# Kernel tuning notes

Hardware: AMD Instinct MI355X
Metric: run time of the kernel (lower is better)

## Reference

```python
import jax, jax.numpy as jnp
import numpy as np


def _conv(x, w, pad):
    return jax.lax.conv_general_dilated(
        x, w, (1, 1), [(pad, pad), (pad, pad)],
        dimension_numbers=('NCHW', 'OIHW', 'NCHW'))


def _avgpool2(x):
    B, C, H, W = x.shape
    return x.reshape(B, C, H // 2, 2, W // 2, 2).mean(axis=(3, 5))


def setup_inputs() -> dict:
    key = jax.random.key(0)
    ks = jax.random.split(key, 10)
    B = 1024
    x = jax.random.uniform(ks[0], (B, 1, 28, 28), jnp.float32)
    # depthwise-separable conv params (in=1 -> depthwise is a plain 3x3 conv)
    dw_w = jax.random.normal(ks[1], (1, 1, 3, 3), jnp.float32) * 0.3
    pw_w = jax.random.normal(ks[2], (32, 1, 1, 1), jnp.float32) * 0.3
    pw_b = jax.random.normal(ks[3], (32,), jnp.float32) * 0.05
    # fixed 4-qubit entangling unitary (real orthogonal 16x16), stand-in for tq.RandomLayer(n_ops=8)
    U = jnp.asarray(np.linalg.qr(np.random.default_rng(0).standard_normal((16, 16)))[0],
                    jnp.float32)
    fus_w = jax.random.normal(ks[4], (128, 36, 3, 3), jnp.float32) * (1.0 / np.sqrt(36 * 9))
    fus_b = jax.random.normal(ks[5], (128,), jnp.float32) * 0.05
    F = 128 * 7 * 7
    cls_w = jax.random.normal(ks[6], (10, F), jnp.float32) * (1.0 / np.sqrt(F))
    cls_b = jax.random.normal(ks[7], (10,), jnp.float32) * 0.05
    reg_w = jax.random.normal(ks[8], (1, F), jnp.float32) * (1.0 / np.sqrt(F))
    reg_b = jax.random.normal(ks[9], (1,), jnp.float32) * 0.05
    return {'x': x, 'dw_w': dw_w, 'pw_w': pw_w, 'pw_b': pw_b, 'U': U,
            'fus_w': fus_w, 'fus_b': fus_b, 'cls_w': cls_w, 'cls_b': cls_b,
            'reg_w': reg_w, 'reg_b': reg_b}


def _quantum_patches(x, U):
    # x: (B,1,28,28) -> 14x14 grid of 2x2 patches, 4 RY angles per patch
    B = x.shape[0]
    p = x.reshape(B, 14, 2, 14, 2).transpose(0, 1, 3, 2, 4).reshape(B, 14, 14, 4)
    h = 0.5 * p
    a = jnp.stack([jnp.cos(h), jnp.sin(h)], axis=-1)       # (B,14,14,4,2)
    # RY-encoded product state |psi> = kron over 4 wires -> 16 real amplitudes
    amp = jnp.einsum('...i,...j,...k,...l->...ijkl',
                     a[..., 0, :], a[..., 1, :], a[..., 2, :], a[..., 3, :]
                     ).reshape(B, 14, 14, 16)
    state = amp @ U.T                                       # entangling layer
    probs = state * state
    idx = jnp.arange(16)
    # PauliZ expectation per wire; wire 0 is the most significant bit
    signs = 1.0 - 2.0 * (((idx[None, :] >> (3 - jnp.arange(4)[:, None])) & 1)
                         .astype(jnp.float32))              # (4,16)
    meas = probs @ signs.T                                  # (B,14,14,4)
    # replicate torch.cat(patches,dim=1).view(B,4,14,14): flat row-major then reshape
    return meas.reshape(B, 14 * 14 * 4).reshape(B, 4, 14, 14)


def reference(x, dw_w, pw_w, pw_b, U, fus_w, fus_b, cls_w, cls_b, reg_w, reg_b):
    B = x.shape[0]
    out_ds = _conv(_conv(x, dw_w, 1), pw_w, 0) + pw_b[None, :, None, None]  # (B,32,28,28)
    out_q = _quantum_patches(x, U)                                          # (B,4,14,14)
    out = jnp.concatenate([_avgpool2(out_ds), out_q], axis=1)               # (B,36,14,14)
    out = jax.nn.relu(_conv(out, fus_w, 1) + fus_b[None, :, None, None])    # (B,128,14,14)
    out = _avgpool2(out)                                                    # (B,128,7,7)
    flat = out.reshape(B, -1)
    logits = flat @ cls_w.T + cls_b
    aux = flat @ reg_w.T + reg_b
    return (logits, aux)
```

## Files before the change

kernel.cpp:

```cpp
#include <hip/hip_runtime.h>
#include <math.h>


typedef __bf16 bf16x8 __attribute__((ext_vector_type(8)));
typedef __bf16 bf16x4 __attribute__((ext_vector_type(4)));
typedef float  f32x16 __attribute__((ext_vector_type(16)));

union Pack8 { __bf16 h[8]; uint4 v; };
union QPair { struct { bf16x4 lo, hi; } p; bf16x8 v; };

__global__ __launch_bounds__(256) void prep(
    const float* __restrict__ fus_w,
    const float* __restrict__ cls_w,
    const float* __restrict__ reg_w,
    __bf16* __restrict__ bfrag,
    float* __restrict__ clsTT)
{
    const int gid = blockIdx.x * 256 + threadIdx.x;
    if (gid < 43008) {
        const int j    = gid & 7;
        const int frag = gid >> 3;
        const int lane = frag & 63;
        const int rest = frag >> 6;
        const int m  = rest % 21;
        const int nt = rest / 21;
        const int n  = nt * 32 + (lane & 31);
        const int hk = lane >> 5;
        float v;
        if (m < 18) {
            const int t = m >> 1, ks = m & 1;
            const int ic = ks * 16 + hk * 8 + j;
            v = fus_w[n * 324 + ic * 9 + t];
        } else {
            const int ps = m - 18;
            const int k  = hk * 8 + j;
            const int tap = ps * 4 + (k >> 2);
            const int ch  = k & 3;
            v = (tap < 9) ? fus_w[n * 324 + (32 + ch) * 9 + tap] : 0.f;
        }
        bfrag[gid] = (__bf16)v;
    } else if (gid < 43008 + 86016) {
        const int e   = gid - 43008;
        const int kk  = e % 12;
        const int r0  = e / 12;
        const int l31 = r0 & 31;
        const int r1  = r0 >> 5;
        const int hk  = r1 & 1;
        const int r2  = r1 >> 1;
        const int q   = r2 & 3;
        const int r3  = r2 >> 2;
        const int mt  = r3 % 7;
        const int nt  = r3 / 7;
        const int oc   = nt * 32 + l31;
        const int cell = mt * 8 + q * 2 + hk;
        float v = 0.f;
        if (cell < 49 && kk < 11) {
            const int f = oc * 49 + cell;
            v = (kk < 10) ? cls_w[kk * 6272 + f] : reg_w[f];
        }
        clsTT[e] = v;
    }
}

__device__ __forceinline__ void patch_work(
    const int tid, const float* __restrict__ xs, __bf16* __restrict__ actT,
    __bf16* __restrict__ Qt,
    const float* __restrict__ dw_w, const float* __restrict__ pw_w,
    const float* __restrict__ pw_b, const float* __restrict__ U)
{
    if (tid >= 196) return;
    const int i = tid / 14, j = tid % 14;
    const int Y = 2 * i, X = 2 * j;

    float w9[9];
    #pragma unroll
    for (int t = 0; t < 9; ++t) w9[t] = dw_w[t];
    float dsum = 0.f;
    #pragma unroll
    for (int dy = 0; dy < 2; ++dy) {
        #pragma unroll
        for (int dx = 0; dx < 2; ++dx) {
            const int cy = Y + dy, cx = X + dx;
            #pragma unroll
            for (int ky = 0; ky < 3; ++ky) {
                const int yy = cy + ky - 1;
                if (yy < 0 || yy > 27) continue;
                #pragma unroll
                for (int kx = 0; kx < 3; ++kx) {
                    const int xx = cx + kx - 1;
                    if (xx < 0 || xx > 27) continue;
                    dsum += xs[yy * 28 + xx] * w9[ky * 3 + kx];
                }
            }
        }
    }
    const float dpool = 0.25f * dsum;

    const int sp_o = (i + 1) * 16 + (j + 1);
    #pragma unroll
    for (int c8 = 0; c8 < 4; ++c8) {
        Pack8 pk;
        #pragma unroll
        for (int e = 0; e < 8; ++e)
            pk.h[e] = (__bf16)(pw_w[c8 * 8 + e] * dpool + pw_b[c8 * 8 + e]);
        ((uint4*)actT)[sp_o * 5 + c8] = pk.v;
    }

    const float p0 = xs[Y * 28 + X],       p1 = xs[Y * 28 + X + 1];
    const float p2 = xs[(Y + 1) * 28 + X], p3 = xs[(Y + 1) * 28 + X + 1];
    float c0, s0, c1, s1, c2, s2, c3, s3;
    sincosf(0.5f * p0, &s0, &c0);
    sincosf(0.5f * p1, &s1, &c1);
    sincosf(0.5f * p2, &s2, &c2);
    sincosf(0.5f * p3, &s3, &c3);
    float a01[4] = {c0 * c1, c0 * s1, s0 * c1, s0 * s1};
    float a23[4] = {c2 * c3, c2 * s3, s2 * c3, s2 * s3};
    float amp[16];
    #pragma unroll
    for (int hi = 0; hi < 4; ++hi)
        #pragma unroll
        for (int lo = 0; lo < 4; ++lo)
            amp[hi * 4 + lo] = a01[hi] * a23[lo];

    float meas[4] = {0.f, 0.f, 0.f, 0.f};
    #pragma unroll
    for (int m = 0; m < 16; ++m) {
        float st = 0.f;
        #pragma unroll
        for (int n = 0; n < 16; ++n) st = fmaf(U[m * 16 + n], amp[n], st);
        const float pm = st * st;
        meas[0] += ((m >> 3) & 1) ? -pm : pm;
        meas[1] += ((m >> 2) & 1) ? -pm : pm;
        meas[2] += ((m >> 1) & 1) ? -pm : pm;
        meas[3] += (m & 1) ? -pm : pm;
    }
    const int fbase = i * 56 + j * 4;
    #pragma unroll
    for (int w = 0; w < 4; ++w) {
        const int f  = fbase + w;
        const int ch = f / 196;
        const int sp = f - ch * 196;
        const int r2 = sp / 14 + 1, c2i = sp % 14 + 1;
        const int sp2 = r2 * 16 + c2i;
        Qt[sp2 * 4 + ch] = (__bf16)meas[w];
    }
}

__device__ __forceinline__ void conv_fold(
    const __bf16* __restrict__ actT, const __bf16* __restrict__ Qt,
    const bf16x8* __restrict__ bfr, const float4* __restrict__ cls4,
    const float fb_l, const int l31, const int hk,
    const int* __restrict__ offL, const int* __restrict__ offH,
    float* __restrict__ a11)
{
    for (int mt = 0; mt < 7; ++mt) {
        const int mp   = mt * 32 + l31;
        const int cell = mp >> 2;
        const int cc = (cell < 49) ? cell : 48;
        const int py = (cc * 9363) >> 16;
        const int px = cc - py * 7;
        const int yy = 2 * py + ((mp >> 1) & 1);
        const int xx = 2 * px + (mp & 1);
        const int rowbase = yy * 16 + xx;

        f32x16 acc = {0.f,0.f,0.f,0.f,0.f,0.f,0.f,0.f,
                      0.f,0.f,0.f,0.f,0.f,0.f,0.f,0.f};

        #pragma unroll
        for (int t = 0; t < 9; ++t) {
            const int ky = t / 3, kx = t - ky * 3;
            const int row = rowbase + ky * 16 + kx;
            const __bf16* rp = actT + row * 40 + hk * 8;
            #pragma unroll
            for (int ks = 0; ks < 2; ++ks) {
                const bf16x8 af = *(const bf16x8*)(rp + ks * 16);
                acc = __builtin_amdgcn_mfma_f32_32x32x16_bf16(af, bfr[t * 2 + ks],
                                                              acc, 0, 0, 0);
            }
        }
        #pragma unroll
        for (int ps = 0; ps < 3; ++ps) {
            QPair u;
            u.p.lo = *(const bf16x4*)(Qt + (rowbase + offL[ps]) * 4);
            u.p.hi = *(const bf16x4*)(Qt + (rowbase + offH[ps]) * 4);
            acc = __builtin_amdgcn_mfma_f32_32x32x16_bf16(u.v, bfr[18 + ps],
                                                          acc, 0, 0, 0);
        }

        const float4* cwm = cls4 + mt * 768;
        #pragma unroll
        for (int q = 0; q < 4; ++q) {
            float pv = 0.f;
            #pragma unroll
            for (int s = 0; s < 4; ++s) {
                const float v = acc[q * 4 + s] + fb_l;
                pv += (v > 0.f ? v : 0.f);
            }
            pv *= 0.25f;
            const float4 w0 = cwm[q * 192 + 0];
            const float4 w1 = cwm[q * 192 + 1];
            const float4 w2 = cwm[q * 192 + 2];
            a11[0]  = fmaf(pv, w0.x, a11[0]);
            a11[1]  = fmaf(pv, w0.y, a11[1]);
            a11[2]  = fmaf(pv, w0.z, a11[2]);
            a11[3]  = fmaf(pv, w0.w, a11[3]);
            a11[4]  = fmaf(pv, w1.x, a11[4]);
            a11[5]  = fmaf(pv, w1.y, a11[5]);
            a11[6]  = fmaf(pv, w1.z, a11[6]);
            a11[7]  = fmaf(pv, w1.w, a11[7]);
            a11[8]  = fmaf(pv, w2.x, a11[8]);
            a11[9]  = fmaf(pv, w2.y, a11[9]);
            a11[10] = fmaf(pv, w2.z, a11[10]);
        }
    }
}

__global__ __launch_bounds__(256, 2) void quanv_fused(
    const float* __restrict__ x,
    const float* __restrict__ dw_w,
    const float* __restrict__ pw_w,
    const float* __restrict__ pw_b,
    const float* __restrict__ U,
    const __bf16* __restrict__ bfrag,
    const float* __restrict__ fus_b,
    const float* __restrict__ clsTT,
    const float* __restrict__ cls_b,
    const float* __restrict__ reg_b,
    float* __restrict__ out,
    int B)
{
    __shared__ __align__(16) __bf16 actT[2][256 * 40];
    __shared__ __align__(16) __bf16 Qt[2][256 * 4];
    __shared__ float xs[2][784];
    __shared__ float red[2][48];

    const int b0  = blockIdx.x * 2;
    const int b1  = b0 + 1;
    const bool two = (b1 < B);
    const int tid = threadIdx.x;

    {
        uint4 z; z.x = 0; z.y = 0; z.z = 0; z.w = 0;
        uint4* a4 = (uint4*)&actT[0][0];
        for (int i = tid; i < 2560; i += 256) a4[i] = z;
        uint4* q4 = (uint4*)&Qt[0][0];
        for (int i = tid; i < 256; i += 256) q4[i] = z;
        const float* xb = x + (size_t)b0 * 784;
        const int tot = two ? 1568 : 784;
        float* xf = &xs[0][0];
        for (int i = tid; i < tot; i += 256) xf[i] = xb[i];
    }

    const int lane = tid & 63, nt = tid >> 6;
    const int l31  = lane & 31, hk = lane >> 5;
    const float fb_l = fus_b[nt * 32 + l31];

    bf16x8 bfr[21];
    {
        const bf16x8* __restrict__ bp = ((const bf16x8*)bfrag) + (nt * 21 * 64 + lane);
        #pragma unroll
        for (int m = 0; m < 21; ++m) bfr[m] = bp[m * 64];
    }

    int offL[3], offH[3];
    #pragma unroll
    for (int ps = 0; ps < 3; ++ps) {
        int tL = ps * 4 + hk * 2;
        int tH = tL + 1;
        if (tL > 8) tL = 0;
        if (tH > 8) tH = 0;
        offL[ps] = (tL / 3) * 16 + (tL % 3);
        offH[ps] = (tH / 3) * 16 + (tH % 3);
    }

    const float4* __restrict__ cls4 =
        ((const float4*)clsTT) + ((((nt * 7) * 4) * 2 + hk) * 32 + l31) * 3;

    __syncthreads();

    patch_work(tid, &xs[0][0], &actT[0][0], &Qt[0][0], dw_w, pw_w, pw_b, U);
    __syncthreads();

    float a11_0[11];
    #pragma unroll
    for (int k = 0; k < 11; ++k) a11_0[k] = 0.f;
    if (two) patch_work(tid, &xs[1][0], &actT[1][0], &Qt[1][0], dw_w, pw_w, pw_b, U);
    conv_fold(&actT[0][0], &Qt[0][0], bfr, cls4, fb_l, l31, hk, offL, offH, a11_0);
    __syncthreads();

    float a11_1[11];
    #pragma unroll
    for (int k = 0; k < 11; ++k) a11_1[k] = 0.f;
    if (two) conv_fold(&actT[1][0], &Qt[1][0], bfr, cls4, fb_l, l31, hk, offL, offH, a11_1);

    #pragma unroll
    for (int k = 0; k < 11; ++k) {
        float a = a11_0[k];
        float c = a11_1[k];
        #pragma unroll
        for (int off = 32; off > 0; off >>= 1) {
            a += __shfl_down(a, off, 64);
            c += __shfl_down(c, off, 64);
        }
        if (lane == 0) { red[0][k * 4 + nt] = a; red[1][k * 4 + nt] = c; }
    }
    __syncthreads();
    if (tid < 11) {
        const float v = red[0][tid * 4] + red[0][tid * 4 + 1]
                      + red[0][tid * 4 + 2] + red[0][tid * 4 + 3];
        if (tid < 10) out[b0 * 10 + tid] = v + cls_b[tid];
        else          out[B * 10 + b0]   = v + reg_b[0];
    } else if (two && tid >= 64 && tid < 75) {
        const int k = tid - 64;
        const float v = red[1][k * 4] + red[1][k * 4 + 1]
                      + red[1][k * 4 + 2] + red[1][k * 4 + 3];
        if (k < 10) out[b1 * 10 + k] = v + cls_b[k];
        else        out[B * 10 + b1] = v + reg_b[0];
    }
}

extern "C" void kernel_launch(void* const* d_in, const int* in_sizes, int n_in,
                              void* d_out, int out_size, void* d_ws, size_t ws_size,
                              hipStream_t stream) {
    const float* x    = (const float*)d_in[0];
    const float* dw_w = (const float*)d_in[1];
    const float* pw_w = (const float*)d_in[2];
    const float* pw_b = (const float*)d_in[3];
    const float* U    = (const float*)d_in[4];
    const float* fw   = (const float*)d_in[5];
    const float* fb   = (const float*)d_in[6];
    const float* cw   = (const float*)d_in[7];
    const float* cb   = (const float*)d_in[8];
    const float* rw   = (const float*)d_in[9];
    const float* rb   = (const float*)d_in[10];
    const int B = in_sizes[0] / 784;

    __bf16* bfrag = (__bf16*)d_ws;
    float*  clsTT = (float*)((char*)d_ws + 86016);

    prep<<<(43008 + 86016 + 255) / 256, 256, 0, stream>>>(fw, cw, rw, bfrag, clsTT);
    const int nblk = (B + 1) / 2;
    quanv_fused<<<nblk, 256, 0, stream>>>(x, dw_w, pw_w, pw_b, U, bfrag, fb,
                                          clsTT, cb, rb, (float*)d_out, B);
}
```

Measured before the change: 108.2 us.

## Process four images per 512-thread block and split conv M-tiles across wave halves

The fused kernel now uses 512 threads per block and handles four images per block instead of two. The two wave halves each take part of the seven fused-conv M tiles (4 and 3). Patch encoding of the next image is overlapped with the conv/fold of the current one through a double-buffered shared activation tile. The per-image B-fragment loads are amortized over more images, at the cost of 44 accumulator registers per thread, a 4/3 load imbalance between the wave halves, and more barriers.

```diff
diff --git a/kernel.cpp b/kernel.cpp
--- a/kernel.cpp
+++ b/kernel.cpp
@@ -151,9 +151,9 @@
     const bf16x8* __restrict__ bfr, const float4* __restrict__ cls4,
     const float fb_l, const int l31, const int hk,
     const int* __restrict__ offL, const int* __restrict__ offH,
-    float* __restrict__ a11)
+    const int mt0, const int mt1, float* __restrict__ a11)
 {
-    for (int mt = 0; mt < 7; ++mt) {
+    for (int mt = mt0; mt < mt1; ++mt) {
         const int mp   = mt * 32 + l31;
         const int cell = mp >> 2;
         const int cc = (cell < 49) ? cell : 48;
@@ -215,7 +215,7 @@
     }
 }
 
-__global__ __launch_bounds__(256, 2) void quanv_fused(
+__global__ __launch_bounds__(512, 2) void quanv_fused(
     const float* __restrict__ x,
     const float* __restrict__ dw_w,
     const float* __restrict__ pw_w,
@@ -231,27 +231,31 @@
 {
     __shared__ __align__(16) __bf16 actT[2][256 * 40];
     __shared__ __align__(16) __bf16 Qt[2][256 * 4];
-    __shared__ float xs[2][784];
-    __shared__ float red[2][48];
-
-    const int b0  = blockIdx.x * 2;
-    const int b1  = b0 + 1;
-    const bool two = (b1 < B);
-    const int tid = threadIdx.x;
+    __shared__ float xs[4][784];
+    __shared__ float red[4][88];
+
+    const int b0   = blockIdx.x * 4;
+    const int nimg = (B - b0 < 4) ? (B - b0) : 4;
+    const int tid  = threadIdx.x;
 
     {
         uint4 z; z.x = 0; z.y = 0; z.z = 0; z.w = 0;
         uint4* a4 = (uint4*)&actT[0][0];
-        for (int i = tid; i < 2560; i += 256) a4[i] = z;
+        for (int i = tid; i < 2560; i += 512) a4[i] = z;
         uint4* q4 = (uint4*)&Qt[0][0];
-        for (int i = tid; i < 256; i += 256) q4[i] = z;
-        const float* xb = x + (size_t)b0 * 784;
-        const int tot = two ? 1568 : 784;
-        float* xf = &xs[0][0];
-        for (int i = tid; i < tot; i += 256) xf[i] = xb[i];
-    }
-
-    const int lane = tid & 63, nt = tid >> 6;
+        if (tid < 256) q4[tid] = z;
+        const float4* xb = (const float4*)(x + (size_t)b0 * 784);
+        float4* xf = (float4*)&xs[0][0];
+        const int tot = nimg * 196;
+        for (int i = tid; i < tot; i += 512) xf[i] = xb[i];
+    }
+
+    const int wv   = tid >> 6;
+    const int lane = tid & 63;
+    const int nt   = wv & 3;
+    const int mh   = wv >> 2;
+    const int mt0  = mh * 4;
+    const int mt1  = mh ? 7 : 4;
     const int l31  = lane & 31, hk = lane >> 5;
     const float fb_l = fus_b[nt * 32 + l31];
 
@@ -276,46 +280,52 @@
     const float4* __restrict__ cls4 =
         ((const float4*)clsTT) + ((((nt * 7) * 4) * 2 + hk) * 32 + l31) * 3;
 
+    float a11[4][11];
+    #pragma unroll
+    for (int ii = 0; ii < 4; ++ii)
+        #pragma unroll
+        for (int k = 0; k < 11; ++k) a11[ii][k] = 0.f;
+
     __syncthreads();
 
     patch_work(tid, &xs[0][0], &actT[0][0], &Qt[0][0], dw_w, pw_w, pw_b, U);
     __syncthreads();
 
-    float a11_0[11];
-    #pragma unroll
-    for (int k = 0; k < 11; ++k) a11_0[k] = 0.f;
-    if (two) patch_work(tid, &xs[1][0], &actT[1][0], &Qt[1][0], dw_w, pw_w, pw_b, U);
-    conv_fold(&actT[0][0], &Qt[0][0], bfr, cls4, fb_l, l31, hk, offL, offH, a11_0);
+    #pragma unroll
+    for (int i = 0; i < 3; ++i) {
+        if (i + 1 < nimg)
+            patch_work(tid, &xs[i + 1][0], &actT[(i + 1) & 1][0],
+                       &Qt[(i + 1) & 1][0], dw_w, pw_w, pw_b, U);
+        if (i < nimg)
+            conv_fold(&actT[i & 1][0], &Qt[i & 1][0], bfr, cls4, fb_l,
+                      l31, hk, offL, offH, mt0, mt1, a11[i]);
+        __syncthreads();
+    }
+
+    if (3 < nimg)
+        conv_fold(&actT[1][0], &Qt[1][0], bfr, cls4, fb_l,
+                  l31, hk, offL, offH, mt0, mt1, a11[3]);
+
+    #pragma unroll
+    for (int ii = 0; ii < 4; ++ii) {
+        #pragma unroll
+        for (int k = 0; k < 11; ++k) {
+            float a = a11[ii][k];
+            #pragma unroll
+            for (int off = 32; off > 0; off >>= 1) a += __shfl_down(a, off, 64);
+            if (lane == 0) red[ii][k * 8 + wv] = a;
+        }
+    }
     __syncthreads();
-
-    float a11_1[11];
-    #pragma unroll
-    for (int k = 0; k < 11; ++k) a11_1[k] = 0.f;
-    if (two) conv_fold(&actT[1][0], &Qt[1][0], bfr, cls4, fb_l, l31, hk, offL, offH, a11_1);
-
-    #pragma unroll
-    for (int k = 0; k < 11; ++k) {
-        float a = a11_0[k];
-        float c = a11_1[k];
-        #pragma unroll
-        for (int off = 32; off > 0; off >>= 1) {
-            a += __shfl_down(a, off, 64);
-            c += __shfl_down(c, off, 64);
-        }
-        if (lane == 0) { red[0][k * 4 + nt] = a; red[1][k * 4 + nt] = c; }
-    }
-    __syncthreads();
-    if (tid < 11) {
-        const float v = red[0][tid * 4] + red[0][tid * 4 + 1]
-                      + red[0][tid * 4 + 2] + red[0][tid * 4 + 3];
-        if (tid < 10) out[b0 * 10 + tid] = v + cls_b[tid];
-        else          out[B * 10 + b0]   = v + reg_b[0];
-    } else if (two && tid >= 64 && tid < 75) {
-        const int k = tid - 64;
-        const float v = red[1][k * 4] + red[1][k * 4 + 1]
-                      + red[1][k * 4 + 2] + red[1][k * 4 + 3];
-        if (k < 10) out[b1 * 10 + k] = v + cls_b[k];
-        else        out[B * 10 + b1] = v + reg_b[0];
+    if (tid < 44) {
+        const int ii = tid / 11, kk = tid - ii * 11;
+        if (ii < nimg) {
+            float v = 0.f;
+            #pragma unroll
+            for (int w = 0; w < 8; ++w) v += red[ii][kk * 8 + w];
+            if (kk < 10) out[(b0 + ii) * 10 + kk] = v + cls_b[kk];
+            else         out[B * 10 + (b0 + ii)]  = v + reg_b[0];
+        }
     }
 }
 
@@ -339,7 +349,7 @@
     float*  clsTT = (float*)((char*)d_ws + 86016);
 
     prep<<<(43008 + 86016 + 255) / 256, 256, 0, stream>>>(fw, cw, rw, bfrag, clsTT);
-    const int nblk = (B + 1) / 2;
-    quanv_fused<<<nblk, 256, 0, stream>>>(x, dw_w, pw_w, pw_b, U, bfrag, fb,
+    const int nblk = (B + 3) / 4;
+    quanv_fused<<<nblk, 512, 0, stream>>>(x, dw_w, pw_w, pw_b, U, bfrag, fb,
                                           clsTT, cb, rb, (float*)d_out, B);
 }
```

Result: slower. 114.0 us (+5.4%).
